# Performance work log

Hardware: AMD Instinct MI355X
Metric: run time of the kernel (lower is better)

Reference implementation:

```python
import jax, jax.numpy as jnp
import numpy as np

D_MODEL = 1024
N_HEADS = 16
D_K = D_MODEL // N_HEADS
LORA_R = 8
SCALING = 16 / 8  # lora_alpha / lora_rank = 2.0


def setup_inputs() -> dict:
    key = jax.random.key(0)
    ks = jax.random.split(key, 12)
    s = 1.0 / np.sqrt(D_MODEL)
    inp = {
        "x": jax.random.normal(ks[0], (4, 2048, D_MODEL), dtype=jnp.float32),
        "w_q": jax.random.normal(ks[1], (D_MODEL, D_MODEL), dtype=jnp.float32) * s,
        "b_q": jnp.zeros((D_MODEL,), dtype=jnp.float32),
        "w_k": jax.random.normal(ks[2], (D_MODEL, D_MODEL), dtype=jnp.float32) * s,
        "b_k": jnp.zeros((D_MODEL,), dtype=jnp.float32),
        "w_v": jax.random.normal(ks[3], (D_MODEL, D_MODEL), dtype=jnp.float32) * s,
        "b_v": jnp.zeros((D_MODEL,), dtype=jnp.float32),
        "w_o": jax.random.normal(ks[4], (D_MODEL, D_MODEL), dtype=jnp.float32) * s,
        "b_o": jnp.zeros((D_MODEL,), dtype=jnp.float32),
        # LoRA: down [d_model -> r], up [r -> d_model]; up init nonzero here so grads flow
        "a_q": jax.random.normal(ks[5], (D_MODEL, LORA_R), dtype=jnp.float32) * s,
        "u_q": jax.random.normal(ks[6], (LORA_R, D_MODEL), dtype=jnp.float32) * 0.01,
        "a_k": jax.random.normal(ks[7], (D_MODEL, LORA_R), dtype=jnp.float32) * s,
        "u_k": jax.random.normal(ks[8], (LORA_R, D_MODEL), dtype=jnp.float32) * 0.01,
        "a_v": jax.random.normal(ks[9], (D_MODEL, LORA_R), dtype=jnp.float32) * s,
        "u_v": jax.random.normal(ks[10], (LORA_R, D_MODEL), dtype=jnp.float32) * 0.01,
    }
    return inp


def reference(x, w_q, b_q, w_k, b_k, w_v, b_v, w_o, b_o, a_q, u_q, a_k, u_k, a_v, u_v):
    B, S, D = x.shape
    # base projections + LoRA (eval mode: dropout off)
    q = x @ w_q + b_q + (x @ a_q) @ u_q * SCALING
    k = x @ w_k + b_k + (x @ a_k) @ u_k * SCALING
    v = x @ w_v + b_v + (x @ a_v) @ u_v * SCALING
    # [B, H, S, d_k]
    q = q.reshape(B, S, N_HEADS, D_K).transpose(0, 2, 1, 3)
    k = k.reshape(B, S, N_HEADS, D_K).transpose(0, 2, 1, 3)
    v = v.reshape(B, S, N_HEADS, D_K).transpose(0, 2, 1, 3)
    scores = jnp.einsum("bhsd,bhtd->bhst", q, k) / np.sqrt(D_K)
    probs = jax.nn.softmax(scores, axis=-1)
    out = jnp.einsum("bhst,bhtd->bhsd", probs, v)
    out = out.transpose(0, 2, 1, 3).reshape(B, S, D)
    return out @ w_o + b_o
```

## Files before the change

### kernel.cpp

```cpp
#include <hip/hip_runtime.h>
#include <stdint.h>

typedef unsigned short u16;
typedef unsigned int u32;
typedef __bf16 bf16x8 __attribute__((ext_vector_type(8)));
typedef __bf16 bf16x4 __attribute__((ext_vector_type(4)));
typedef float f32x4 __attribute__((ext_vector_type(4)));
typedef float f32x16 __attribute__((ext_vector_type(16)));
typedef u32 u32x4 __attribute__((ext_vector_type(4)));

#define SEQ 2048
#define QSCALE 0.1803368801111137f

__device__ __forceinline__ float fast_exp2(float x) { return __builtin_amdgcn_exp2f(x); }

__device__ __forceinline__ void async16(const void* g, void* l) {
  __builtin_amdgcn_global_load_lds((const __attribute__((address_space(1))) void*)g,
                                   (__attribute__((address_space(3))) void*)l, 16, 0, 0);
}

__device__ __forceinline__ u32 pkbf(float a, float b) {
  u16 xa = __builtin_bit_cast(u16, (__bf16)a);
  u16 xb = __builtin_bit_cast(u16, (__bf16)b);
  return (u32)xa | ((u32)xb << 16);
}


__global__ void prep_all_kernel(const float* __restrict__ x, u16* __restrict__ xb,
                                const float* __restrict__ wq, const float* __restrict__ wk,
                                const float* __restrict__ wv, const float* __restrict__ wo,
                                const float* __restrict__ aq, const float* __restrict__ ak,
                                const float* __restrict__ av,
                                const float* __restrict__ uq, const float* __restrict__ uk,
                                const float* __restrict__ uv,
                                u16* __restrict__ weffT,
                                const float* __restrict__ bq, const float* __restrict__ bk,
                                const float* __restrict__ bv, float* __restrict__ bias_qkv) {
  __shared__ float wt[32][33];
  __shared__ float at[32][8];
  __shared__ float ut[8][33];
  const int bid = blockIdx.x;
  const int t = threadIdx.x;
  if (bid < 8192) {
    int i = (bid * 256 + t) * 4;
    float4 v = *(const float4*)(x + i);
    bf16x4 o;
    o[0] = (__bf16)v.x; o[1] = (__bf16)v.y; o[2] = (__bf16)v.z; o[3] = (__bf16)v.w;
    *(bf16x4*)(xb + i) = o;
  } else if (bid < 12288) {
    const int p = (bid - 8192) >> 10, bx = (bid - 8192) & 1023;
    const int tn0 = (bx & 31) * 32, tk0 = (bx >> 5) * 32;
    const float* w = (p == 0) ? wq : (p == 1) ? wk : (p == 2) ? wv : wo;
    const float* a = (p == 0) ? aq : (p == 1) ? ak : av;
    const float* u = (p == 0) ? uq : (p == 1) ? uk : uv;
    {
      int tk = t >> 3, tn4 = (t & 7) * 4;
      float4 v = *(const float4*)(w + (tk0 + tk) * 1024 + tn0 + tn4);
      wt[tk][tn4] = v.x; wt[tk][tn4 + 1] = v.y; wt[tk][tn4 + 2] = v.z; wt[tk][tn4 + 3] = v.w;
    }
    if (p < 3) {
      at[t >> 3][t & 7] = a[(tk0 + (t >> 3)) * 8 + (t & 7)];
      ut[t >> 5][t & 31] = u[(t >> 5) * 1024 + tn0 + (t & 31)];
    }
    __syncthreads();
    const int tn = t >> 3, tk4 = (t & 7) * 4;
    bf16x4 o;
#pragma unroll
    for (int jj = 0; jj < 4; ++jj) {
      int k = tk4 + jj;
      float val = wt[k][tn];
      if (p < 3) {
        float acc = 0.f;
#pragma unroll
        for (int r = 0; r < 8; ++r) acc += at[k][r] * ut[r][tn];
        val += 2.0f * acc;
      }
      if (p == 0) val *= QSCALE;
      o[jj] = (__bf16)val;
    }
    *(bf16x4*)(weffT + p * 1048576 + (tn0 + tn) * 1024 + tk0 + tk4) = o;
  } else {
    int i = (bid - 12288) * 256 + t;
    bias_qkv[i] = (i < 1024) ? bq[i] * QSCALE : (i < 2048) ? bk[i - 1024] : bv[i - 2048];
  }
}


template <int MODE>
__global__ __launch_bounds__(256, 2)
void gemm_tt(const u16* __restrict__ U, const u16* __restrict__ V, void* __restrict__ OUT,
             u16* __restrict__ vT, const float* __restrict__ bias, const int NU, const int K) {
  __shared__ __align__(16) char smU[8192];
  __shared__ __align__(16) char smV[8192];
  const int t = threadIdx.x;
  const int lane = t & 63, ln = lane & 15, g = lane >> 4, w = t >> 6;
  const int u0 = blockIdx.x * 128, v0 = blockIdx.y * 128;
  const int wu = (w & 1) * 64, wv = (w >> 1) * 64;
  f32x4 acc[4][4] = {};
  for (int k0 = 0; k0 < K; k0 += 32) {
    __syncthreads();
#pragma unroll
    for (int half = 0; half < 2; ++half) {
      int p = half * 256 + t;
      int s = p >> 2, cp = p & 3;
      int c = cp ^ (s & 3);
      int ldsoff = (half * 256 + (t & 192)) * 16;
      async16(U + (u0 + s) * K + k0 + c * 8, smU + ldsoff);
      async16(V + (v0 + s) * K + k0 + c * 8, smV + ldsoff);
    }
    __syncthreads();
    bf16x8 af[4], bf[4];
#pragma unroll
    for (int mt = 0; mt < 4; ++mt)
      af[mt] = *(const bf16x8*)(smU + (wu + mt * 16 + ln) * 64 + ((g ^ (ln & 3)) * 16));
#pragma unroll
    for (int nt = 0; nt < 4; ++nt)
      bf[nt] = *(const bf16x8*)(smV + (wv + nt * 16 + ln) * 64 + ((g ^ (ln & 3)) * 16));
#pragma unroll
    for (int mt = 0; mt < 4; ++mt)
#pragma unroll
      for (int nt = 0; nt < 4; ++nt)
        acc[mt][nt] = __builtin_amdgcn_mfma_f32_16x16x32_bf16(af[mt], bf[nt], acc[mt][nt], 0, 0, 0);
  }
  const bool isV = (MODE == 1) && (u0 + wu >= 2048);
#pragma unroll
  for (int mt = 0; mt < 4; ++mt) {
    const int u = u0 + wu + mt * 16 + g * 4;
    const float4 bs = *(const float4*)(bias + u);
#pragma unroll
    for (int nt = 0; nt < 4; ++nt) {
      const int v = v0 + wv + nt * 16 + ln;
      f32x4 a = acc[mt][nt];
      a[0] += bs.x; a[1] += bs.y; a[2] += bs.z; a[3] += bs.w;
      if (MODE == 0) {
        *(float4*)((float*)OUT + (size_t)v * NU + u) = make_float4(a[0], a[1], a[2], a[3]);
      } else if (!isV) {
        bf16x4 o;
        o[0] = (__bf16)a[0]; o[1] = (__bf16)a[1]; o[2] = (__bf16)a[2]; o[3] = (__bf16)a[3];
        *(bf16x4*)((u16*)OUT + (size_t)v * 2048 + u) = o;
      } else {
        const int uu = u - 2048;
        const int hh = uu >> 6, dd = uu & 63;
        const int bb = v >> 11, ss = v & 2047;
        u16* dst = vT + ((size_t)((bb * 16 + hh) * 64 + dd)) * 2048 + ss;
#pragma unroll
        for (int r = 0; r < 4; ++r)
          *(__bf16*)(dst + (size_t)r * 2048) = (__bf16)a[r];
      }
    }
  }
}


__global__ __launch_bounds__(256, 2)
void attn_kernel(const u16* __restrict__ qkv, const u16* __restrict__ vT,
                 u16* __restrict__ attn_o) {
  __shared__ __align__(16) char smK[32768];
  __shared__ __align__(16) char smVt[32768];
  const int t = threadIdx.x;
  const int lane = t & 63, q32 = lane & 31, hf = lane >> 5, w = t >> 6;
  const int hd = blockIdx.x, qt = blockIdx.y, b = blockIdx.z;
  const int q0 = qt * 256;
  const size_t base_b = (size_t)b * SEQ * 2048;
  const u16* qbase = qkv + base_b + hd * 64;
  const u16* kbase0 = qkv + base_b + 1024 + hd * 64;
  const u16* vbase0 = vT + ((size_t)(b * 16 + hd) * 64) * 2048;

  bf16x8 qf[4][2];
#pragma unroll
  for (int ks = 0; ks < 4; ++ks)
#pragma unroll
    for (int nt = 0; nt < 2; ++nt)
      qf[ks][nt] = *(const bf16x8*)(qbase + (size_t)(q0 + w * 64 + nt * 32 + q32) * 2048 +
                                    ks * 16 + hf * 8);

  bf16x8 ones_frag;
  {
    u32 o2 = (q32 == 0) ? 0x3F803F80u : 0u;
    u32x4 ow = {o2, o2, o2, o2};
    ones_frag = __builtin_bit_cast(bf16x8, ow);
  }

  const u16* srcK[4];
  const u16* srcV[4];
  char* dstK[4];
  char* dstV[4];
#pragma unroll
  for (int i = 0; i < 4; ++i) {
    int p = i * 256 + t;
    {
      int row = p >> 3, cp = p & 7;
      int rowp = (row & ~12) | ((row & 4) << 1) | ((row & 8) >> 1);
      int c = cp ^ (row & 7);
      srcK[i] = kbase0 + (size_t)rowp * 2048 + c * 8;
      dstK[i] = smK + (i * 256 + (t & 192)) * 16;
    }
    {
      int d = p >> 4, cp = p & 15;
      int key = (d & 15) ^ (d >> 3);
      int c = (cp ^ key) & 15;
      srcV[i] = vbase0 + (size_t)d * 2048 + c * 8;
      dstV[i] = smVt + (i * 256 + (t & 192)) * 16;
    }
  }

#pragma unroll
  for (int i = 0; i < 4; ++i) {
    async16(srcK[i], dstK[i]);
    srcK[i] += 128 * 2048;
  }
#pragma unroll
  for (int i = 0; i < 4; ++i) {
    async16(srcV[i], dstV[i]);
    srcV[i] += 128;
  }
  __syncthreads();

  f32x16 accO[2][2] = {};
  f32x16 acc_l[2] = {};

  for (int kt = 0; kt < 16; ++kt) {
    const int cur = kt & 1, nxt = cur ^ 1;
    if (kt < 15) {
#pragma unroll
      for (int i = 0; i < 4; ++i) {
        async16(srcK[i], dstK[i] + nxt * 16384);
        srcK[i] += 128 * 2048;
      }
#pragma unroll
      for (int i = 0; i < 4; ++i) {
        async16(srcV[i], dstV[i] + nxt * 16384);
        srcV[i] += 128;
      }
    }
    const char* kbuf = smK + cur * 16384;
    const char* vbuf = smVt + cur * 16384;

#pragma unroll
    for (int c = 0; c < 4; ++c) {
      f32x16 stc[2] = {};
#pragma unroll
      for (int ks = 0; ks < 4; ++ks) {
        int row = c * 32 + q32;
        bf16x8 kfr = *(const bf16x8*)(kbuf + row * 128 + (((2 * ks + hf) ^ (row & 7)) * 16));
        stc[0] = __builtin_amdgcn_mfma_f32_32x32x16_bf16(kfr, qf[ks][0], stc[0], 0, 0, 0);
        stc[1] = __builtin_amdgcn_mfma_f32_32x32x16_bf16(kfr, qf[ks][1], stc[1], 0, 0, 0);
      }
#pragma unroll
      for (int kh = 0; kh < 2; ++kh) {
        bf16x8 pfrag[2];
#pragma unroll
        for (int nt = 0; nt < 2; ++nt) {
          float e[8];
#pragma unroll
          for (int j = 0; j < 8; ++j) e[j] = fast_exp2(stc[nt][8 * kh + j]);
          u32x4 bw;
          bw[0] = pkbf(e[0], e[1]);
          bw[1] = pkbf(e[2], e[3]);
          bw[2] = pkbf(e[4], e[5]);
          bw[3] = pkbf(e[6], e[7]);
          pfrag[nt] = __builtin_bit_cast(bf16x8, bw);
          acc_l[nt] = __builtin_amdgcn_mfma_f32_32x32x16_bf16(ones_frag, pfrag[nt], acc_l[nt], 0, 0, 0);
        }
#pragma unroll
        for (int mt = 0; mt < 2; ++mt) {
          int row = mt * 32 + q32;
          int key = (row & 15) ^ (row >> 3);
          bf16x8 vfr = *(const bf16x8*)(vbuf + row * 256 +
                                        (((4 * c + 2 * kh + hf) ^ key) & 15) * 16);
          accO[mt][0] = __builtin_amdgcn_mfma_f32_32x32x16_bf16(vfr, pfrag[0], accO[mt][0], 0, 0, 0);
          accO[mt][1] = __builtin_amdgcn_mfma_f32_32x32x16_bf16(vfr, pfrag[1], accO[mt][1], 0, 0, 0);
        }
      }
    }
    if (kt < 15) __syncthreads();
  }

#pragma unroll
  for (int nt = 0; nt < 2; ++nt) {
    float lv = __shfl(acc_l[nt][0], q32);
    float il = 1.0f / lv;
    const int s = q0 + w * 64 + nt * 32 + q32;
#pragma unroll
    for (int mt = 0; mt < 2; ++mt)
#pragma unroll
      for (int qd = 0; qd < 4; ++qd) {
        int d0 = 32 * mt + 8 * qd + 4 * hf;
        bf16x4 o;
#pragma unroll
        for (int r = 0; r < 4; ++r) o[r] = (__bf16)(accO[mt][nt][4 * qd + r] * il);
        *(bf16x4*)(attn_o + (size_t)(b * SEQ + s) * 1024 + hd * 64 + d0) = o;
      }
  }
}


extern "C" void kernel_launch(void* const* d_in, const int* in_sizes, int n_in,
                              void* d_out, int out_size, void* d_ws, size_t ws_size,
                              hipStream_t stream) {
  const float* x  = (const float*)d_in[0];
  const float* wq = (const float*)d_in[1];
  const float* bq = (const float*)d_in[2];
  const float* wk = (const float*)d_in[3];
  const float* bk = (const float*)d_in[4];
  const float* wv = (const float*)d_in[5];
  const float* bv = (const float*)d_in[6];
  const float* wo = (const float*)d_in[7];
  const float* bo = (const float*)d_in[8];
  const float* aq = (const float*)d_in[9];
  const float* uq = (const float*)d_in[10];
  const float* ak = (const float*)d_in[11];
  const float* uk = (const float*)d_in[12];
  const float* av = (const float*)d_in[13];
  const float* uv = (const float*)d_in[14];

  char* ws = (char*)d_ws;
  u16* xb       = (u16*)(ws);
  u16* attn_o   = (u16*)(ws);
  u16* qkv      = (u16*)(ws + (16u << 20));
  u16* vT       = (u16*)(ws + (48u << 20));
  u16* weffT    = (u16*)(ws + (64u << 20));
  float* biasq  = (float*)(ws + (72u << 20));

  prep_all_kernel<<<dim3(12300), dim3(256), 0, stream>>>(
      x, xb, wq, wk, wv, wo, aq, ak, av, uq, uk, uv, weffT, bq, bk, bv, biasq);
  gemm_tt<1><<<dim3(24, 64), dim3(256), 0, stream>>>(weffT, xb, (void*)qkv, vT, biasq, 2048, 1024);
  attn_kernel<<<dim3(16, 8, 4), dim3(256), 0, stream>>>(qkv, vT, attn_o);
  gemm_tt<0><<<dim3(8, 64), dim3(256), 0, stream>>>(weffT + 3u * 1048576u, attn_o, d_out, nullptr, bo, 1024, 1024);
}
```

Baseline: 298.0 us.

## Double-buffer GEMM LDS tiles with K=64 steps and 32x32 MFMA

Rewrites the projection GEMM main loop to double-buffer the LDS tiles, prefetching the next K-slice with async global-to-LDS loads while computing the current one. The K step grows from 32 to 64, which halves the number of barrier-separated iterations. The MFMA shape changes from 16x16x32 to 32x32x16, which lowers the LDS fragment reads per FLOP. LDS use rises from 16KB to 64KB per block, which may limit occupancy to the two blocks per CU requested by the launch bounds.

```diff
diff --git a/kernel.cpp b/kernel.cpp
--- a/kernel.cpp
+++ b/kernel.cpp
@@ -90,62 +90,113 @@
 __global__ __launch_bounds__(256, 2)
 void gemm_tt(const u16* __restrict__ U, const u16* __restrict__ V, void* __restrict__ OUT,
              u16* __restrict__ vT, const float* __restrict__ bias, const int NU, const int K) {
-  __shared__ __align__(16) char smU[8192];
-  __shared__ __align__(16) char smV[8192];
+  __shared__ __align__(16) char smU[32768];
+  __shared__ __align__(16) char smV[32768];
   const int t = threadIdx.x;
-  const int lane = t & 63, ln = lane & 15, g = lane >> 4, w = t >> 6;
+  const int lane = t & 63, q32 = lane & 31, hf = lane >> 5, w = t >> 6;
   const int u0 = blockIdx.x * 128, v0 = blockIdx.y * 128;
   const int wu = (w & 1) * 64, wv = (w >> 1) * 64;
-  f32x4 acc[4][4] = {};
-  for (int k0 = 0; k0 < K; k0 += 32) {
-    __syncthreads();
-#pragma unroll
-    for (int half = 0; half < 2; ++half) {
-      int p = half * 256 + t;
-      int s = p >> 2, cp = p & 3;
-      int c = cp ^ (s & 3);
-      int ldsoff = (half * 256 + (t & 192)) * 16;
-      async16(U + (u0 + s) * K + k0 + c * 8, smU + ldsoff);
-      async16(V + (v0 + s) * K + k0 + c * 8, smV + ldsoff);
-    }
-    __syncthreads();
-    bf16x8 af[4], bf[4];
-#pragma unroll
-    for (int mt = 0; mt < 4; ++mt)
-      af[mt] = *(const bf16x8*)(smU + (wu + mt * 16 + ln) * 64 + ((g ^ (ln & 3)) * 16));
-#pragma unroll
-    for (int nt = 0; nt < 4; ++nt)
-      bf[nt] = *(const bf16x8*)(smV + (wv + nt * 16 + ln) * 64 + ((g ^ (ln & 3)) * 16));
-#pragma unroll
-    for (int mt = 0; mt < 4; ++mt)
-#pragma unroll
-      for (int nt = 0; nt < 4; ++nt)
-        acc[mt][nt] = __builtin_amdgcn_mfma_f32_16x16x32_bf16(af[mt], bf[nt], acc[mt][nt], 0, 0, 0);
-  }
+
+  const u16* srcU[4];
+  const u16* srcV[4];
+  char* dstU[4];
+  char* dstV[4];
+#pragma unroll
+  for (int i = 0; i < 4; ++i) {
+    int p = i * 256 + t;
+    int row = p >> 3, cp = p & 7, c = cp ^ (row & 7);
+    srcU[i] = U + (size_t)(u0 + row) * K + c * 8;
+    srcV[i] = V + (size_t)(v0 + row) * K + c * 8;
+    char* d = (char*)(size_t)((i * 256 + (t & 192)) * 16);
+    dstU[i] = smU + (size_t)d;
+    dstV[i] = smV + (size_t)d;
+  }
+
+#pragma unroll
+  for (int i = 0; i < 4; ++i) {
+    async16(srcU[i], dstU[i]);
+    srcU[i] += 64;
+  }
+#pragma unroll
+  for (int i = 0; i < 4; ++i) {
+    async16(srcV[i], dstV[i]);
+    srcV[i] += 64;
+  }
+  __syncthreads();
+
+  f32x16 acc[2][2] = {};
+  const int NIT = K >> 6;
+  for (int it = 0; it < NIT; ++it) {
+    const int cur = it & 1, nxt = cur ^ 1;
+    if (it < NIT - 1) {
+#pragma unroll
+      for (int i = 0; i < 4; ++i) {
+        async16(srcU[i], dstU[i] + nxt * 16384);
+        srcU[i] += 64;
+      }
+#pragma unroll
+      for (int i = 0; i < 4; ++i) {
+        async16(srcV[i], dstV[i] + nxt * 16384);
+        srcV[i] += 64;
+      }
+    }
+    const char* ub = smU + cur * 16384;
+    const char* vb = smV + cur * 16384;
+    bf16x8 af[4][2], bf[4][2];
+#pragma unroll
+    for (int ks = 0; ks < 4; ++ks) {
+#pragma unroll
+      for (int mt = 0; mt < 2; ++mt) {
+        int row = wu + mt * 32 + q32;
+        af[ks][mt] = *(const bf16x8*)(ub + row * 128 + (((2 * ks + hf) ^ (row & 7)) * 16));
+      }
+#pragma unroll
+      for (int nt = 0; nt < 2; ++nt) {
+        int row = wv + nt * 32 + q32;
+        bf[ks][nt] = *(const bf16x8*)(vb + row * 128 + (((2 * ks + hf) ^ (row & 7)) * 16));
+      }
+    }
+#pragma unroll
+    for (int ks = 0; ks < 4; ++ks)
+#pragma unroll
+      for (int mt = 0; mt < 2; ++mt)
+#pragma unroll
+        for (int nt = 0; nt < 2; ++nt)
+          acc[mt][nt] = __builtin_amdgcn_mfma_f32_32x32x16_bf16(af[ks][mt], bf[ks][nt],
+                                                               acc[mt][nt], 0, 0, 0);
+    if (it < NIT - 1) __syncthreads();
+  }
+
   const bool isV = (MODE == 1) && (u0 + wu >= 2048);
 #pragma unroll
-  for (int mt = 0; mt < 4; ++mt) {
-    const int u = u0 + wu + mt * 16 + g * 4;
-    const float4 bs = *(const float4*)(bias + u);
-#pragma unroll
-    for (int nt = 0; nt < 4; ++nt) {
-      const int v = v0 + wv + nt * 16 + ln;
-      f32x4 a = acc[mt][nt];
-      a[0] += bs.x; a[1] += bs.y; a[2] += bs.z; a[3] += bs.w;
-      if (MODE == 0) {
-        *(float4*)((float*)OUT + (size_t)v * NU + u) = make_float4(a[0], a[1], a[2], a[3]);
-      } else if (!isV) {
-        bf16x4 o;
-        o[0] = (__bf16)a[0]; o[1] = (__bf16)a[1]; o[2] = (__bf16)a[2]; o[3] = (__bf16)a[3];
-        *(bf16x4*)((u16*)OUT + (size_t)v * 2048 + u) = o;
-      } else {
-        const int uu = u - 2048;
-        const int hh = uu >> 6, dd = uu & 63;
-        const int bb = v >> 11, ss = v & 2047;
-        u16* dst = vT + ((size_t)((bb * 16 + hh) * 64 + dd)) * 2048 + ss;
-#pragma unroll
-        for (int r = 0; r < 4; ++r)
-          *(__bf16*)(dst + (size_t)r * 2048) = (__bf16)a[r];
+  for (int mt = 0; mt < 2; ++mt) {
+#pragma unroll
+    for (int rq = 0; rq < 4; ++rq) {
+      const int u = u0 + wu + mt * 32 + 8 * rq + 4 * hf;
+      const float4 bs = *(const float4*)(bias + u);
+#pragma unroll
+      for (int nt = 0; nt < 2; ++nt) {
+        const int v = v0 + wv + nt * 32 + q32;
+        float a0 = acc[mt][nt][4 * rq + 0] + bs.x;
+        float a1 = acc[mt][nt][4 * rq + 1] + bs.y;
+        float a2 = acc[mt][nt][4 * rq + 2] + bs.z;
+        float a3 = acc[mt][nt][4 * rq + 3] + bs.w;
+        if (MODE == 0) {
+          *(float4*)((float*)OUT + (size_t)v * NU + u) = make_float4(a0, a1, a2, a3);
+        } else if (!isV) {
+          bf16x4 o;
+          o[0] = (__bf16)a0; o[1] = (__bf16)a1; o[2] = (__bf16)a2; o[3] = (__bf16)a3;
+          *(bf16x4*)((u16*)OUT + (size_t)v * 2048 + u) = o;
+        } else {
+          const int uu = u - 2048;
+          const int hh = uu >> 6, dd = uu & 63;
+          const int bb = v >> 11, ss = v & 2047;
+          u16* dst = vT + ((size_t)((bb * 16 + hh) * 64 + dd)) * 2048 + ss;
+          *(__bf16*)(dst) = (__bf16)a0;
+          *(__bf16*)(dst + 2048) = (__bf16)a1;
+          *(__bf16*)(dst + 4096) = (__bf16)a2;
+          *(__bf16*)(dst + 6144) = (__bf16)a3;
+        }
       }
     }
   }
```

Result: no change. 303.8 us (+1.9%).
